# Kernel optimization log

Hardware: AMD Instinct MI355X
Metric: run time of the kernel (lower is better)

## Reference

```python
import jax, jax.numpy as jnp
import numpy as np

B, K, C, D, L, H, FF = 64, 1024, 512, 256, 2, 4, 1024
DH = D // H
EPS = 1e-5
NEG = -jnp.inf
SCALE = 1.0 / float(np.sqrt(DH))


def _ln(x, w, b):
    m = x.mean(-1, keepdims=True)
    v = ((x - m) ** 2).mean(-1, keepdims=True)
    return (x - m) * jax.lax.rsqrt(v + EPS) * w + b


def _star_attn(x, key_pad, pad_c, Wq, bq, Wk, bk, Wv, bv, Wo, bo):
    # Star topology: rows 0,1 (query,dustbin) attend to all non-padded keys;
    # each candidate row attends only to {query, dustbin, itself}.
    Bb, S, _ = x.shape
    q = (x @ Wq.T + bq).reshape(Bb, S, H, DH)
    k = (x @ Wk.T + bk).reshape(Bb, S, H, DH)
    v = (x @ Wv.T + bv).reshape(Bb, S, H, DH)
    # global rows
    qg = q[:, :2]
    sg = jnp.einsum('bthd,bshd->bhts', qg, k) * SCALE            # [B,H,2,S]
    sg = jnp.where(key_pad[:, None, None, :], NEG, sg)
    out_g = jnp.einsum('bhts,bshd->bthd', jax.nn.softmax(sg, -1), v)  # [B,2,H,DH]
    # candidate rows: scores against the 2 global keys + self key
    qc, kc, vc = q[:, 2:], k[:, 2:], v[:, 2:]
    kg, vg = k[:, :2], v[:, :2]
    s2 = jnp.einsum('bkhd,bthd->bkht', qc, kg) * SCALE           # [B,K,H,2]
    ss = jnp.einsum('bkhd,bkhd->bkh', qc, kc) * SCALE            # [B,K,H]
    ss = jnp.where(pad_c[:, :, None], NEG, ss)                   # padded self-key disallowed
    w = jax.nn.softmax(jnp.concatenate([s2, ss[..., None]], -1), -1)  # [B,K,H,3]
    out_c = jnp.einsum('bkht,bthd->bkhd', w[..., :2], vg) + w[..., 2:] * vc
    out = jnp.concatenate([out_g, out_c], 1).reshape(Bb, S, D)
    return out @ Wo.T + bo


def _forward(query, candidates, candidate_mask, qp_w, qp_b, cp_w, cp_b,
             dustbin, type_emb, ln1_w, ln1_b, ln2_w, ln2_b,
             Wq, bq, Wk, bk, Wv, bv, Wo, bo,
             ff1_w, ff1_b, ff2_w, ff2_b, head_ln_w, head_ln_b, head_w, head_b):
    Bb = query.shape[0]
    qt = (query @ qp_w.T + qp_b + type_emb[0])[:, None]          # [B,1,D]
    dt = jnp.broadcast_to(dustbin + type_emb[1], (Bb, 1, D))
    ct = candidates @ cp_w.T + cp_b + type_emb[2]                # [B,K,D]
    x = jnp.concatenate([qt, dt, ct], 1)                         # [B,K+2,D]
    pad_c = jnp.logical_not(candidate_mask)
    key_pad = jnp.concatenate([jnp.zeros((Bb, 2), bool), pad_c], 1)
    for l in range(L):  # pre-LN encoder layers (norm_first, eval so dropout=0)
        x = x + _star_attn(_ln(x, ln1_w[l], ln1_b[l]), key_pad, pad_c,
                           Wq[l], bq[l], Wk[l], bk[l], Wv[l], bv[l], Wo[l], bo[l])
        h = _ln(x, ln2_w[l], ln2_b[l])
        x = x + (jax.nn.gelu(h @ ff1_w[l].T + ff1_b[l], approximate=False) @ ff2_w[l].T + ff2_b[l])
    logits = (_ln(x, head_ln_w, head_ln_b) @ head_w.T + head_b)[..., 0]  # [B,K+2]
    cand = jnp.where(candidate_mask, logits[:, 2:], NEG)
    return jnp.concatenate([logits[:, 1:2], cand], 1)            # [B,K+1]


def setup_inputs() -> dict:
    key = jax.random.key(0)
    ks = iter(jax.random.split(key, 40))
    n = lambda shape, s=0.02: jax.random.normal(next(ks), shape, jnp.float32) * s
    return dict(
        query=jax.random.normal(next(ks), (B, C), jnp.float32),
        candidates=jax.random.normal(next(ks), (B, K, C), jnp.float32),
        candidate_mask=jax.random.bernoulli(next(ks), 0.9, (B, K)),
        qp_w=n((D, C)), qp_b=jnp.zeros(D),
        cp_w=n((D, C)), cp_b=jnp.zeros(D),
        dustbin=n((D,)), type_emb=n((3, D)),
        ln1_w=jnp.ones((L, D)), ln1_b=jnp.zeros((L, D)),
        ln2_w=jnp.ones((L, D)), ln2_b=jnp.zeros((L, D)),
        Wq=n((L, D, D)), bq=jnp.zeros((L, D)),
        Wk=n((L, D, D)), bk=jnp.zeros((L, D)),
        Wv=n((L, D, D)), bv=jnp.zeros((L, D)),
        Wo=n((L, D, D)), bo=jnp.zeros((L, D)),
        ff1_w=n((L, FF, D)), ff1_b=jnp.zeros((L, FF)),
        ff2_w=n((L, D, FF)), ff2_b=jnp.zeros((L, D)),
        head_ln_w=jnp.ones(D), head_ln_b=jnp.zeros(D),
        head_w=n((1, D)), head_b=jnp.zeros(1),
    )


def reference(query, candidates, candidate_mask, qp_w, qp_b, cp_w, cp_b,
              dustbin, type_emb, ln1_w, ln1_b, ln2_w, ln2_b,
              Wq, bq, Wk, bk, Wv, bv, Wo, bo,
              ff1_w, ff1_b, ff2_w, ff2_b, head_ln_w, head_ln_b, head_w, head_b):
    return _forward(query, candidates, candidate_mask, qp_w, qp_b, cp_w, cp_b,
                    dustbin, type_emb, ln1_w, ln1_b, ln2_w, ln2_b,
                    Wq, bq, Wk, bk, Wv, bv, Wo, bo,
                    ff1_w, ff1_b, ff2_w, ff2_b, head_ln_w, head_ln_b, head_w, head_b)
```

## Files before the change

kernel.cpp:

```cpp
#include <hip/hip_runtime.h>
#include <math.h>

static constexpr int Bc = 64;
static constexpr int Kc = 1024;
static constexpr int Cc = 512;
static constexpr int Dc = 256;
static constexpr int Hc = 4;
static constexpr int Sc = 1026;
static constexpr int FFc = 1024;
static constexpr float EPSc = 1e-5f;
static constexpr float SCALEc = 0.125f;
static constexpr float NEG_OUT = -1.0e30f;

typedef __attribute__((ext_vector_type(8))) short short8;
typedef __attribute__((ext_vector_type(8))) unsigned short u16x8;
typedef __attribute__((ext_vector_type(4))) float f32x4;

__device__ __forceinline__ float bf2f(unsigned short u) {
  union { float f; unsigned int i; } c; c.i = ((unsigned int)u) << 16; return c.f;
}
__device__ __forceinline__ unsigned short f2bf(float f) {
  union { float f; unsigned int i; } c; c.f = f;
  unsigned int i = c.i;
  unsigned int r = (i + 0x7fffu + ((i >> 16) & 1u)) >> 16;
  return (unsigned short)r;
}

__device__ __forceinline__ float wave_sum(float v) {
#pragma unroll
  for (int off = 32; off > 0; off >>= 1) v += __shfl_xor(v, off, 64);
  return v;
}
__device__ __forceinline__ float wave_max(float v) {
#pragma unroll
  for (int off = 32; off > 0; off >>= 1) v = fmaxf(v, __shfl_xor(v, off, 64));
  return v;
}

__device__ __forceinline__ void async_ld16(const unsigned short* g, unsigned short* l) {
  __builtin_amdgcn_global_load_lds(
      (const __attribute__((address_space(1))) void*)g,
      (__attribute__((address_space(3))) void*)l, 16, 0, 0);
}

__device__ __forceinline__ float gelu_fast(float u) {
  const float z = 1.5957691216057308f * u * (1.0f + 0.044715f * u * u);
  return u / (1.0f + __expf(-z));
}

template <int EPI, int MAP, int CASTA>
__global__ __launch_bounds__(256) void gemm_mfma(
    const void* __restrict__ Av, const unsigned short* __restrict__ W,
    const float* __restrict__ bias, const void* extra,
    void* Cout, int N, int Kd, int ldc, int MB, int NB) {
  __shared__ unsigned short lds[16384];
  const int xcd = blockIdx.x & 7;
  const int slot = blockIdx.x >> 3;
  const int nb = slot % NB;
  const int mb = (slot / NB) * 8 + xcd;
  if (mb >= MB) return;
  const int m0 = mb * 128;
  const int n0 = nb * 128;
  const int tid = threadIdx.x;
  const int w = tid >> 6;
  const int lane = tid & 63;

  const unsigned short* A = (const unsigned short*)Av;
  const float* Af = (const float*)Av;

  const int srA[2] = {(w * 2 + 0) * 16 + (lane >> 2), (w * 2 + 1) * 16 + (lane >> 2)};
  const unsigned short* pA[2];
  const unsigned short* pB[2];
#pragma unroll
  for (int c = 0; c < 2; ++c) {
    const int kc = ((lane & 3) ^ ((srA[c] >> 1) & 3)) * 8;
    if (!CASTA) pA[c] = A + (size_t)(m0 + srA[c]) * Kd + kc;
    pB[c] = W + (size_t)(n0 + srA[c]) * Kd + kc;
  }
  const int lreg0 = (w * 2 + 0) * 512;
  const int lreg1 = (w * 2 + 1) * 512;

  f32x4 zero = {0.f, 0.f, 0.f, 0.f};
  f32x4 acc[4][4];
#pragma unroll
  for (int i = 0; i < 4; ++i)
#pragma unroll
    for (int j = 0; j < 4; ++j) acc[i][j] = zero;

  const int mrow = (w & 1) * 64;
  const int nrow = (w >> 1) * 64;
  const int l15 = lane & 15;
  const int quad = lane >> 4;
  const int koff = (quad ^ ((l15 >> 1) & 3)) * 16;

  auto stage = [&](int kk, int b) {
    if (CASTA) {
#pragma unroll
      for (int wi = 0; wi < 4; ++wi) {
        const int g = wi * 256 + tid;
        const int row = g >> 3;
        const int k4 = g & 7;
        const int phys =
            row * 32 + ((((k4 >> 1) ^ ((row >> 1) & 3))) << 3) + ((k4 & 1) << 2);
        const float4 a4 =
            *(const float4*)(Af + (size_t)(m0 + row) * Kd + kk + k4 * 4);
        ushort4 o;
        o.x = f2bf(a4.x); o.y = f2bf(a4.y); o.z = f2bf(a4.z); o.w = f2bf(a4.w);
        *(ushort4*)(&lds[b * 4096 + phys]) = o;
      }
    } else {
      async_ld16(pA[0] + kk, &lds[b * 4096 + lreg0]);
      async_ld16(pA[1] + kk, &lds[b * 4096 + lreg1]);
    }
    async_ld16(pB[0] + kk, &lds[8192 + b * 4096 + lreg0]);
    async_ld16(pB[1] + kk, &lds[8192 + b * 4096 + lreg1]);
  };

  const int niter = Kd >> 5;
  stage(0, 0);
  for (int it = 0; it < niter; ++it) {
    const int cur = it & 1;
    __syncthreads();
    if (it + 1 < niter) stage((it + 1) << 5, cur ^ 1);
    const char* AsB = (const char*)&lds[cur * 4096];
    const char* WsB = (const char*)&lds[8192 + cur * 4096];
    short8 af[4], bfr[4];
#pragma unroll
    for (int i = 0; i < 4; ++i)
      af[i] = *(const short8*)(AsB + (size_t)(mrow + i * 16 + l15) * 64 + koff);
#pragma unroll
    for (int j = 0; j < 4; ++j)
      bfr[j] = *(const short8*)(WsB + (size_t)(nrow + j * 16 + l15) * 64 + koff);
#pragma unroll
    for (int i = 0; i < 4; ++i)
#pragma unroll
      for (int j = 0; j < 4; ++j)
        acc[i][j] = __builtin_amdgcn_mfma_f32_16x16x32_bf16(af[i], bfr[j],
                                                            acc[i][j], 0, 0, 0);
  }

  const float* extraF = (const float*)extra;
  const unsigned short* extraB = (const unsigned short*)extra;
  float bj[4];
#pragma unroll
  for (int j = 0; j < 4; ++j) {
    const int n = n0 + nrow + j * 16 + l15;
    bj[j] = bias[n];
    if (EPI == 1) bj[j] += extraF[n];
  }
  __syncthreads();
#pragma unroll
  for (int i = 0; i < 4; ++i) {
    const int rbase = mrow + i * 16 + quad * 4;
#pragma unroll
    for (int r = 0; r < 4; ++r) {
#pragma unroll
      for (int j = 0; j < 4; ++j) {
        float v = acc[i][j][r] + bj[j];
        if (EPI == 3) v = gelu_fast(v);
        lds[(rbase + r) * 128 + nrow + j * 16 + l15] = f2bf(v);
      }
    }
  }
  __syncthreads();
  unsigned short* outb = (unsigned short*)Cout;
#pragma unroll
  for (int c = 0; c < 8; ++c) {
    const int idx = c * 256 + tid;
    const int row = idx >> 4;
    const int col = (idx & 15) * 8;
    const int m = m0 + row;
    const size_t orow =
        (MAP == 1) ? ((size_t)(m >> 10) * Sc + 2 + (m & 1023)) : (size_t)m;
    const size_t go = orow * (size_t)ldc + n0 + col;
    u16x8 val = *(const u16x8*)(&lds[row * 128 + col]);
    if (EPI == 2) {
      u16x8 rv = *(const u16x8*)(extraB + go);
#pragma unroll
      for (int e = 0; e < 8; ++e) val[e] = f2bf(bf2f(val[e]) + bf2f(rv[e]));
    }
    *(u16x8*)(outb + go) = val;
  }
}

struct CastTab {
  const float* src[10];
  unsigned short* dst[10];
  int n4[10];
};
__global__ __launch_bounds__(256) void cast_multi(CastTab t) {
  const int e = blockIdx.y;
  const int n4 = t.n4[e];
  const float4* s = (const float4*)t.src[e];
  ushort4* d = (ushort4*)t.dst[e];
  for (int i = blockIdx.x * 256 + threadIdx.x; i < n4; i += gridDim.x * 256) {
    float4 f = s[i];
    ushort4 o;
    o.x = f2bf(f.x); o.y = f2bf(f.y); o.z = f2bf(f.z); o.w = f2bf(f.w);
    d[i] = o;
  }
}

__global__ __launch_bounds__(256) void bias_concat(const float* bq, const float* bk,
                                                   const float* bv, float* qkvb) {
  const int i = blockIdx.x * 256 + threadIdx.x;
  if (i >= 2 * 768) return;
  const int l = i / 768;
  const int j = i - l * 768;
  float v;
  if (j < 256) v = bq[l * 256 + j];
  else if (j < 512) v = bk[l * 256 + j - 256];
  else v = bv[l * 256 + j - 512];
  qkvb[i] = v;
}

__global__ __launch_bounds__(256) void embed_qd(
    const float* __restrict__ qin, const float* __restrict__ qp_w,
    const float* __restrict__ qp_b, const float* __restrict__ dustbin,
    const float* __restrict__ type_emb, unsigned short* __restrict__ x) {
  const int b = blockIdx.x;
  const int d = threadIdx.x;
  __shared__ __align__(16) float qs[512];
  qs[d] = qin[b * 512 + d];
  qs[d + 256] = qin[b * 512 + 256 + d];
  __syncthreads();
  float acc = 0.0f;
  const float* wr = qp_w + (size_t)d * 512;
#pragma unroll 4
  for (int c = 0; c < 512; c += 4) {
    float4 w4 = *(const float4*)(wr + c);
    acc = fmaf(qs[c], w4.x, acc);
    acc = fmaf(qs[c + 1], w4.y, acc);
    acc = fmaf(qs[c + 2], w4.z, acc);
    acc = fmaf(qs[c + 3], w4.w, acc);
  }
  const size_t base = (size_t)b * Sc * Dc;
  x[base + d] = f2bf(acc + qp_b[d] + type_emb[d]);
  x[base + Dc + d] = f2bf(dustbin[d] + type_emb[Dc + d]);
}

__global__ __launch_bounds__(256) void ln_kernel(
    const unsigned short* __restrict__ x, const float* __restrict__ w,
    const float* __restrict__ b, unsigned short* __restrict__ y, int nrows) {
  const int wave = threadIdx.x >> 6;
  const int lane = threadIdx.x & 63;
  const int row = blockIdx.x * 4 + wave;
  if (row >= nrows) return;
  const unsigned short* xr = x + (size_t)row * Dc;
  ushort4 xv = *(const ushort4*)(xr + lane * 4);
  const float v0 = bf2f(xv.x), v1 = bf2f(xv.y), v2 = bf2f(xv.z), v3 = bf2f(xv.w);
  float s = v0 + v1 + v2 + v3;
  float sq = v0 * v0 + v1 * v1 + v2 * v2 + v3 * v3;
  s = wave_sum(s);
  sq = wave_sum(sq);
  const float mean = s * (1.0f / Dc);
  const float var = sq * (1.0f / Dc) - mean * mean;
  const float rs = rsqrtf(var + EPSc);
  float4 wv = *(const float4*)(w + lane * 4);
  float4 bv = *(const float4*)(b + lane * 4);
  ushort4 o;
  o.x = f2bf((v0 - mean) * rs * wv.x + bv.x);
  o.y = f2bf((v1 - mean) * rs * wv.y + bv.y);
  o.z = f2bf((v2 - mean) * rs * wv.z + bv.z);
  o.w = f2bf((v3 - mean) * rs * wv.w + bv.w);
  *(ushort4*)(y + (size_t)row * Dc + lane * 4) = o;
}

__global__ __launch_bounds__(256) void attn_global(
    const unsigned short* __restrict__ qkv, const unsigned char* __restrict__ mask,
    unsigned short* __restrict__ ao) {
  const int b = blockIdx.x;
  const int h = blockIdx.y;
  const int tid = threadIdx.x;
  const int wv = tid >> 6;
  const int lane = tid & 63;
  __shared__ float q0s[64], q1s[64];
  __shared__ float sc0[Sc], sc1[Sc];
  __shared__ float rbuf[4][2];
  __shared__ float obuf[2][4][64];
  const size_t base = (size_t)b * Sc * 768 + h * 64;
  if (tid < 64) {
    q0s[tid] = bf2f(qkv[base + tid]);
    q1s[tid] = bf2f(qkv[base + 768 + tid]);
  }
  __syncthreads();

  float lm0 = -INFINITY, lm1 = -INFINITY;
  for (int s = tid; s < Sc; s += 256) {
    const unsigned short* kr = qkv + base + 256 + (size_t)s * 768;
    float d0 = 0.0f, d1 = 0.0f;
#pragma unroll
    for (int c = 0; c < 64; c += 8) {
      u16x8 kv = *(const u16x8*)(kr + c);
#pragma unroll
      for (int e = 0; e < 8; ++e) {
        const float kf = bf2f(kv[e]);
        d0 = fmaf(q0s[c + e], kf, d0);
        d1 = fmaf(q1s[c + e], kf, d1);
      }
    }
    const bool pad = (s >= 2) && (mask[b * Kc + (s - 2)] == 0);
    const float s0 = pad ? -INFINITY : d0 * SCALEc;
    const float s1 = pad ? -INFINITY : d1 * SCALEc;
    sc0[s] = s0; sc1[s] = s1;
    lm0 = fmaxf(lm0, s0); lm1 = fmaxf(lm1, s1);
  }
  lm0 = wave_max(lm0);
  lm1 = wave_max(lm1);
  if (lane == 0) { rbuf[wv][0] = lm0; rbuf[wv][1] = lm1; }
  __syncthreads();
  const float m0 = fmaxf(fmaxf(rbuf[0][0], rbuf[1][0]), fmaxf(rbuf[2][0], rbuf[3][0]));
  const float m1 = fmaxf(fmaxf(rbuf[0][1], rbuf[1][1]), fmaxf(rbuf[2][1], rbuf[3][1]));
  float ls0 = 0.0f, ls1 = 0.0f;
  for (int s = tid; s < Sc; s += 256) {
    const float e0 = expf(sc0[s] - m0);
    const float e1 = expf(sc1[s] - m1);
    sc0[s] = e0; sc1[s] = e1;
    ls0 += e0; ls1 += e1;
  }
  ls0 = wave_sum(ls0);
  ls1 = wave_sum(ls1);
  __syncthreads();
  if (lane == 0) { rbuf[wv][0] = ls0; rbuf[wv][1] = ls1; }
  __syncthreads();
  const float t0 = rbuf[0][0] + rbuf[1][0] + rbuf[2][0] + rbuf[3][0];
  const float t1 = rbuf[0][1] + rbuf[1][1] + rbuf[2][1] + rbuf[3][1];
  float o0 = 0.0f, o1 = 0.0f;
  for (int s = wv; s < Sc; s += 4) {
    const float vvv = bf2f(qkv[base + 512 + (size_t)s * 768 + lane]);
    o0 = fmaf(sc0[s], vvv, o0);
    o1 = fmaf(sc1[s], vvv, o1);
  }
  obuf[0][wv][lane] = o0;
  obuf[1][wv][lane] = o1;
  __syncthreads();
  if (wv == 0) {
    const float a0 = obuf[0][0][lane] + obuf[0][1][lane] + obuf[0][2][lane] + obuf[0][3][lane];
    const float a1 = obuf[1][0][lane] + obuf[1][1][lane] + obuf[1][2][lane] + obuf[1][3][lane];
    const size_t ob = ((size_t)b * Sc) * Dc + h * 64;
    ao[ob + lane] = f2bf(a0 / t0);
    ao[ob + Dc + lane] = f2bf(a1 / t1);
  }
}

__global__ __launch_bounds__(256) void attn_cand(
    const unsigned short* __restrict__ qkv, const unsigned char* __restrict__ mask,
    unsigned short* __restrict__ ao) {
  const int bk = blockIdx.x;
  const int b = bk >> 10;
  const int kk = bk & 1023;
  const int h = threadIdx.x >> 6;
  const int lane = threadIdx.x & 63;
  const size_t rowg = (size_t)b * Sc * 768 + h * 64;
  const size_t rowc = rowg + (size_t)(2 + kk) * 768;
  const float qc = bf2f(qkv[rowc + lane]);
  float p0 = qc * bf2f(qkv[rowg + 256 + lane]);
  float p1 = qc * bf2f(qkv[rowg + 256 + 768 + lane]);
  float p2 = qc * bf2f(qkv[rowc + 256 + lane]);
#pragma unroll
  for (int off = 32; off > 0; off >>= 1) {
    p0 += __shfl_xor(p0, off, 64);
    p1 += __shfl_xor(p1, off, 64);
    p2 += __shfl_xor(p2, off, 64);
  }
  const bool pad = (mask[b * Kc + kk] == 0);
  const float s0 = p0 * SCALEc;
  const float s1 = p1 * SCALEc;
  const float s2 = pad ? -INFINITY : p2 * SCALEc;
  const float m = fmaxf(fmaxf(s0, s1), s2);
  const float e0 = expf(s0 - m);
  const float e1 = expf(s1 - m);
  const float e2 = pad ? 0.0f : expf(s2 - m);
  const float inv = 1.0f / (e0 + e1 + e2);
  const float o = (e0 * bf2f(qkv[rowg + 512 + lane]) +
                   e1 * bf2f(qkv[rowg + 512 + 768 + lane]) +
                   e2 * bf2f(qkv[rowc + 512 + lane])) * inv;
  ao[((size_t)b * Sc + 2 + kk) * Dc + h * 64 + lane] = f2bf(o);
}

__global__ __launch_bounds__(256) void head_kernel(
    const unsigned short* __restrict__ x, const float* __restrict__ lnw,
    const float* __restrict__ lnb, const float* __restrict__ hw,
    const float* __restrict__ hb, const unsigned char* __restrict__ mask,
    float* __restrict__ out) {
  const int gw = blockIdx.x * 4 + (threadIdx.x >> 6);
  const int lane = threadIdx.x & 63;
  if (gw >= Bc * 1025) return;
  const int b = gw / 1025;
  const int j = gw - b * 1025;
  const int s = 1 + j;
  const unsigned short* xr = x + ((size_t)b * Sc + s) * Dc;
  ushort4 xv = *(const ushort4*)(xr + lane * 4);
  const float v0 = bf2f(xv.x), v1 = bf2f(xv.y), v2 = bf2f(xv.z), v3 = bf2f(xv.w);
  float su = v0 + v1 + v2 + v3;
  float sq = v0 * v0 + v1 * v1 + v2 * v2 + v3 * v3;
  su = wave_sum(su);
  sq = wave_sum(sq);
  const float mean = su * (1.0f / Dc);
  const float var = sq * (1.0f / Dc) - mean * mean;
  const float rs = rsqrtf(var + EPSc);
  float4 wv = *(const float4*)(lnw + lane * 4);
  float4 bv = *(const float4*)(lnb + lane * 4);
  float4 hv = *(const float4*)(hw + lane * 4);
  float d = ((v0 - mean) * rs * wv.x + bv.x) * hv.x +
            ((v1 - mean) * rs * wv.y + bv.y) * hv.y +
            ((v2 - mean) * rs * wv.z + bv.z) * hv.z +
            ((v3 - mean) * rs * wv.w + bv.w) * hv.w;
  d = wave_sum(d);
  if (lane == 0) {
    const float logit = d + hb[0];
    float res;
    if (j == 0) res = logit;
    else res = (mask[b * Kc + (j - 1)] != 0) ? logit : NEG_OUT;
    out[(size_t)b * 1025 + j] = res;
  }
}

extern "C" void kernel_launch(void* const* d_in, const int* in_sizes, int n_in,
                              void* d_out, int out_size, void* d_ws,
                              size_t ws_size, hipStream_t stream) {
  const float* query = (const float*)d_in[0];
  const float* cands = (const float*)d_in[1];
  const unsigned char* mask = (const unsigned char*)d_in[2];
  const float* qp_w = (const float*)d_in[3];
  const float* qp_b = (const float*)d_in[4];
  const float* cp_w = (const float*)d_in[5];
  const float* cp_b = (const float*)d_in[6];
  const float* dustbin = (const float*)d_in[7];
  const float* type_emb = (const float*)d_in[8];
  const float* ln1_w = (const float*)d_in[9];
  const float* ln1_b = (const float*)d_in[10];
  const float* ln2_w = (const float*)d_in[11];
  const float* ln2_b = (const float*)d_in[12];
  const float* Wq = (const float*)d_in[13];
  const float* bq = (const float*)d_in[14];
  const float* Wk = (const float*)d_in[15];
  const float* bk = (const float*)d_in[16];
  const float* Wv = (const float*)d_in[17];
  const float* bv = (const float*)d_in[18];
  const float* Wo = (const float*)d_in[19];
  const float* bo = (const float*)d_in[20];
  const float* f1w = (const float*)d_in[21];
  const float* f1b = (const float*)d_in[22];
  const float* f2w = (const float*)d_in[23];
  const float* f2b = (const float*)d_in[24];
  const float* hlw = (const float*)d_in[25];
  const float* hlb = (const float*)d_in[26];
  const float* hw = (const float*)d_in[27];
  const float* hb = (const float*)d_in[28];
  float* out = (float*)d_out;

  const size_t XSZ = (size_t)Bc * Sc * Dc;
  const size_t FFSZ = (size_t)Bc * Sc * FFc;

  char* p = (char*)d_ws;
  unsigned short* x = (unsigned short*)p;   p += XSZ * 2;
  unsigned short* y = (unsigned short*)p;   p += XSZ * 2;
  unsigned short* ao = (unsigned short*)p;  p += XSZ * 2;
  unsigned short* big = (unsigned short*)p; p += FFSZ * 2;
  unsigned short* qkv = big;
  unsigned short* ff = big;
  unsigned short* cpw_b = (unsigned short*)p;
  unsigned short* qkvw_b = cpw_b + 131072;
  unsigned short* Wo_b = qkvw_b + 2 * 768 * 256;
  unsigned short* f1_b = Wo_b + 131072;
  unsigned short* f2_b = f1_b + 524288;
  float* qkvb = (float*)(f2_b + 524288);

  const int BS = Bc * Sc;
  auto sgrid = [](int MB, int NB) { return (unsigned)(NB * (((MB + 7) >> 3) << 3)); };

  CastTab t;
  t.src[0] = cp_w;  t.dst[0] = cpw_b; t.n4[0] = 131072 / 4;
  t.src[1] = Wo;    t.dst[1] = Wo_b;  t.n4[1] = 131072 / 4;
  t.src[2] = f1w;   t.dst[2] = f1_b;  t.n4[2] = 524288 / 4;
  t.src[3] = f2w;   t.dst[3] = f2_b;  t.n4[3] = 524288 / 4;
  for (int l = 0; l < 2; ++l) {
    t.src[4 + l * 3 + 0] = Wq + l * 65536;
    t.src[4 + l * 3 + 1] = Wk + l * 65536;
    t.src[4 + l * 3 + 2] = Wv + l * 65536;
    t.dst[4 + l * 3 + 0] = qkvw_b + l * 196608 + 0 * 65536;
    t.dst[4 + l * 3 + 1] = qkvw_b + l * 196608 + 1 * 65536;
    t.dst[4 + l * 3 + 2] = qkvw_b + l * 196608 + 2 * 65536;
    t.n4[4 + l * 3 + 0] = 65536 / 4;
    t.n4[4 + l * 3 + 1] = 65536 / 4;
    t.n4[4 + l * 3 + 2] = 65536 / 4;
  }
  cast_multi<<<dim3(128, 10), 256, 0, stream>>>(t);
  bias_concat<<<6, 256, 0, stream>>>(bq, bk, bv, qkvb);

  gemm_mfma<1, 1, 1><<<sgrid(512, 2), 256, 0, stream>>>(
      cands, cpw_b, cp_b, type_emb + 2 * Dc, x, Dc, Cc, Dc, 512, 2);
  embed_qd<<<Bc, 256, 0, stream>>>(query, qp_w, qp_b, dustbin, type_emb, x);

  for (int l = 0; l < 2; ++l) {
    ln_kernel<<<BS / 4, 256, 0, stream>>>(x, ln1_w + l * Dc, ln1_b + l * Dc, y, BS);
    gemm_mfma<4, 0, 0><<<sgrid(513, 6), 256, 0, stream>>>(
        y, qkvw_b + l * 196608, qkvb + l * 768, nullptr, qkv, 768, Dc, 768, 513, 6);
    attn_global<<<dim3(Bc, Hc), 256, 0, stream>>>(qkv, mask, ao);
    attn_cand<<<Bc * Kc, 256, 0, stream>>>(qkv, mask, ao);
    gemm_mfma<2, 0, 0><<<sgrid(513, 2), 256, 0, stream>>>(
        ao, Wo_b + l * 65536, bo + l * Dc, x, x, Dc, Dc, Dc, 513, 2);
    ln_kernel<<<BS / 4, 256, 0, stream>>>(x, ln2_w + l * Dc, ln2_b + l * Dc, y, BS);
    gemm_mfma<3, 0, 0><<<sgrid(513, 8), 256, 0, stream>>>(
        y, f1_b + l * 524288 / 2, f1b + l * FFc, nullptr, ff, FFc, Dc, FFc, 513, 8);
    gemm_mfma<2, 0, 0><<<sgrid(513, 2), 256, 0, stream>>>(
        ff, f2_b + l * 524288 / 2, f2b + l * Dc, x, x, Dc, FFc, Dc, 513, 2);
  }

  head_kernel<<<(Bc * 1025 + 3) / 4, 256, 0, stream>>>(x, hlw, hlb, hw, hb, mask, out);
}
```

Baseline: 1.002 ms.

## Transpose MFMA operands for packed epilogue stores and use hardware bf16 pack conversion

```diff
diff --git a/kernel.cpp b/kernel.cpp
--- a/kernel.cpp
+++ b/kernel.cpp
@@ -24,6 +24,11 @@
   unsigned int i = c.i;
   unsigned int r = (i + 0x7fffu + ((i >> 16) & 1u)) >> 16;
   return (unsigned short)r;
+}
+__device__ __forceinline__ unsigned int cvt_pk_bf16(float a, float b) {
+  unsigned int d;
+  asm("v_cvt_pk_bf16_f32 %0, %1, %2" : "=v"(d) : "v"(a), "v"(b));
+  return d;
 }
 
 __device__ __forceinline__ float wave_sum(float v) {
@@ -104,9 +109,10 @@
             row * 32 + ((((k4 >> 1) ^ ((row >> 1) & 3))) << 3) + ((k4 & 1) << 2);
         const float4 a4 =
             *(const float4*)(Af + (size_t)(m0 + row) * Kd + kk + k4 * 4);
-        ushort4 o;
-        o.x = f2bf(a4.x); o.y = f2bf(a4.y); o.z = f2bf(a4.z); o.w = f2bf(a4.w);
-        *(ushort4*)(&lds[b * 4096 + phys]) = o;
+        uint2 o;
+        o.x = cvt_pk_bf16(a4.x, a4.y);
+        o.y = cvt_pk_bf16(a4.z, a4.w);
+        *(uint2*)(&lds[b * 4096 + phys]) = o;
       }
     } else {
       async_ld16(pA[0] + kk, &lds[b * 4096 + lreg0]);
@@ -135,49 +141,68 @@
     for (int i = 0; i < 4; ++i)
 #pragma unroll
       for (int j = 0; j < 4; ++j)
-        acc[i][j] = __builtin_amdgcn_mfma_f32_16x16x32_bf16(af[i], bfr[j],
+        acc[i][j] = __builtin_amdgcn_mfma_f32_16x16x32_bf16(bfr[j], af[i],
                                                             acc[i][j], 0, 0, 0);
   }
 
   const float* extraF = (const float*)extra;
   const unsigned short* extraB = (const unsigned short*)extra;
-  float bj[4];
+  float4 bj[4];
 #pragma unroll
   for (int j = 0; j < 4; ++j) {
-    const int n = n0 + nrow + j * 16 + l15;
-    bj[j] = bias[n];
-    if (EPI == 1) bj[j] += extraF[n];
+    const int n = n0 + nrow + j * 16 + quad * 4;
+    float4 t4 = *(const float4*)(bias + n);
+    if (EPI == 1) {
+      const float4 e4 = *(const float4*)(extraF + n);
+      t4.x += e4.x; t4.y += e4.y; t4.z += e4.z; t4.w += e4.w;
+    }
+    bj[j] = t4;
   }
   __syncthreads();
 #pragma unroll
   for (int i = 0; i < 4; ++i) {
-    const int rbase = mrow + i * 16 + quad * 4;
-#pragma unroll
-    for (int r = 0; r < 4; ++r) {
-#pragma unroll
-      for (int j = 0; j < 4; ++j) {
-        float v = acc[i][j][r] + bj[j];
-        if (EPI == 3) v = gelu_fast(v);
-        lds[(rbase + r) * 128 + nrow + j * 16 + l15] = f2bf(v);
+    const int m = mrow + i * 16 + l15;
+    const int swz = (m & 7) << 1;
+#pragma unroll
+    for (int j = 0; j < 4; ++j) {
+      float v0 = acc[i][j][0] + bj[j].x;
+      float v1 = acc[i][j][1] + bj[j].y;
+      float v2 = acc[i][j][2] + bj[j].z;
+      float v3 = acc[i][j][3] + bj[j].w;
+      if (EPI == 3) {
+        v0 = gelu_fast(v0); v1 = gelu_fast(v1);
+        v2 = gelu_fast(v2); v3 = gelu_fast(v3);
       }
+      uint2 pk;
+      pk.x = cvt_pk_bf16(v0, v1);
+      pk.y = cvt_pk_bf16(v2, v3);
+      const int g = ((nrow + j * 16 + quad * 4) >> 2) ^ swz;
+      *(uint2*)(&lds[m * 128 + g * 4]) = pk;
     }
   }
   __syncthreads();
   unsigned short* outb = (unsigned short*)Cout;
 #pragma unroll
-  for (int c = 0; c < 8; ++c) {
-    const int idx = c * 256 + tid;
+  for (int c8 = 0; c8 < 8; ++c8) {
+    const int idx = c8 * 256 + tid;
     const int row = idx >> 4;
-    const int col = (idx & 15) * 8;
+    const int cc = idx & 15;
+    const int gsr = (2 * cc) ^ ((row & 7) << 1);
+    u16x8 val = *(const u16x8*)(&lds[row * 128 + gsr * 4]);
+    const int col = cc * 8;
     const int m = m0 + row;
     const size_t orow =
         (MAP == 1) ? ((size_t)(m >> 10) * Sc + 2 + (m & 1023)) : (size_t)m;
     const size_t go = orow * (size_t)ldc + n0 + col;
-    u16x8 val = *(const u16x8*)(&lds[row * 128 + col]);
     if (EPI == 2) {
       u16x8 rv = *(const u16x8*)(extraB + go);
-#pragma unroll
-      for (int e = 0; e < 8; ++e) val[e] = f2bf(bf2f(val[e]) + bf2f(rv[e]));
+      unsigned int* vp = (unsigned int*)&val;
+#pragma unroll
+      for (int e = 0; e < 4; ++e) {
+        const float a0 = bf2f(val[2 * e]) + bf2f(rv[2 * e]);
+        const float a1 = bf2f(val[2 * e + 1]) + bf2f(rv[2 * e + 1]);
+        vp[e] = cvt_pk_bf16(a0, a1);
+      }
     }
     *(u16x8*)(outb + go) = val;
   }
@@ -192,11 +217,12 @@
   const int e = blockIdx.y;
   const int n4 = t.n4[e];
   const float4* s = (const float4*)t.src[e];
-  ushort4* d = (ushort4*)t.dst[e];
+  uint2* d = (uint2*)t.dst[e];
   for (int i = blockIdx.x * 256 + threadIdx.x; i < n4; i += gridDim.x * 256) {
     float4 f = s[i];
-    ushort4 o;
-    o.x = f2bf(f.x); o.y = f2bf(f.y); o.z = f2bf(f.z); o.w = f2bf(f.w);
+    uint2 o;
+    o.x = cvt_pk_bf16(f.x, f.y);
+    o.y = cvt_pk_bf16(f.z, f.w);
     d[i] = o;
   }
 }
@@ -258,12 +284,12 @@
   const float rs = rsqrtf(var + EPSc);
   float4 wv = *(const float4*)(w + lane * 4);
   float4 bv = *(const float4*)(b + lane * 4);
-  ushort4 o;
-  o.x = f2bf((v0 - mean) * rs * wv.x + bv.x);
-  o.y = f2bf((v1 - mean) * rs * wv.y + bv.y);
-  o.z = f2bf((v2 - mean) * rs * wv.z + bv.z);
-  o.w = f2bf((v3 - mean) * rs * wv.w + bv.w);
-  *(ushort4*)(y + (size_t)row * Dc + lane * 4) = o;
+  uint2 o;
+  o.x = cvt_pk_bf16((v0 - mean) * rs * wv.x + bv.x,
+                    (v1 - mean) * rs * wv.y + bv.y);
+  o.y = cvt_pk_bf16((v2 - mean) * rs * wv.z + bv.z,
+                    (v3 - mean) * rs * wv.w + bv.w);
+  *(uint2*)(y + (size_t)row * Dc + lane * 4) = o;
 }
 
 __global__ __launch_bounds__(256) void attn_global(
```

Result: slower. 1.037 ms (+3.4%).
